# Kernel optimization log

Measured on AMD Instinct MI355X. Metric: run time of the kernel, lower is better.

The kernel has to match this reference:

```python
import jax, jax.numpy as jnp
import numpy as np

B, S, A, H, NH = 4, 4096, 512, 1024, 16
HD = H // NH  # 64


def setup_inputs() -> dict:
    key = jax.random.key(0)
    ks = jax.random.split(key, 12)
    s = 1.0 / np.sqrt(H)
    return {
        "hidden_states": jax.random.normal(ks[0], (B, S, H), jnp.float32),
        "audio_tokens": jax.random.normal(ks[1], (B, A, H), jnp.float32),
        "attention_mask": jax.random.randint(ks[2], (B, A), 0, 2, jnp.int32),
        "Wq": jax.random.normal(ks[3], (H, H), jnp.float32) * s,
        "bq": jnp.zeros((H,), jnp.float32),
        "Wk": jax.random.normal(ks[4], (H, H), jnp.float32) * s,
        "bk": jnp.zeros((H,), jnp.float32),
        "Wv": jax.random.normal(ks[5], (H, H), jnp.float32) * s,
        "bv": jnp.zeros((H,), jnp.float32),
        "Wo": jax.random.normal(ks[6], (H, H), jnp.float32) * s,
        "bo": jnp.zeros((H,), jnp.float32),
        "ln_gamma": jnp.ones((H,), jnp.float32),
        "ln_beta": jnp.zeros((H,), jnp.float32),
        "residual_scale": jnp.asarray(0.05, jnp.float32),
    }


def _san(x, big=10000.0):
    return jnp.nan_to_num(x, nan=0.0, posinf=big, neginf=-big)


def reference(hidden_states, audio_tokens, attention_mask, Wq, bq, Wk, bk, Wv, bv,
              Wo, bo, ln_gamma, ln_beta, residual_scale):
    hs = _san(hidden_states).astype(jnp.float32)
    at = _san(audio_tokens).astype(jnp.float32)

    def heads(x, W, b):  # [b, t, H] -> [b, t, nh, hd]
        return _san(x @ W.T + b).reshape(x.shape[0], x.shape[1], NH, HD)

    q = heads(hs, Wq, bq)            # [B,S,NH,HD]
    k = heads(at, Wk, bk)            # [B,A,NH,HD]
    v = heads(at, Wv, bv)            # [B,A,NH,HD]

    scale = max(np.sqrt(HD), 1e-8)
    scores = jnp.einsum("bsnd,band->bnsa", q, k) / scale  # [B,NH,S,A]
    scores = jnp.clip(_san(jnp.clip(scores, -50.0, 50.0), 50.0), -50.0, 50.0)

    attend = (attention_mask > 0)[:, None, None, :]       # [B,1,1,A]
    scores = jnp.where(attend, scores, -10000.0)
    scores = jnp.clip(scores, -50.0, 50.0)

    probs = jax.nn.softmax(scores, axis=-1)
    probs = _san(probs, 1.0)
    probs = probs / (jnp.sum(probs, axis=-1, keepdims=True) + 1e-8)

    ctx = jnp.einsum("bnsa,band->bsnd", probs, v).reshape(B, S, H)
    delta = _san(ctx @ Wo.T + bo)

    rs = jnp.clip(residual_scale, 0.0, 0.3)
    delta = rs * delta

    mu = jnp.mean(delta, axis=-1, keepdims=True)
    var = jnp.mean(jnp.square(delta - mu), axis=-1, keepdims=True)
    delta = (delta - mu) / jnp.sqrt(var + 1e-5) * ln_gamma + ln_beta
    return delta
```

## Files before the change

kernel.cpp:

```cpp
#include <hip/hip_runtime.h>
#include <hip/hip_bf16.h>
#include <cstdint>
#include <cstddef>

#define B_  4
#define S_  4096
#define A_  512
#define H_  1024
#define NH_ 16
#define HD_ 64

typedef __bf16 bf16;
typedef __bf16 bf16x8 __attribute__((ext_vector_type(8)));
typedef __bf16 bf16x4 __attribute__((ext_vector_type(4)));
typedef float  fx4    __attribute__((ext_vector_type(4)));

typedef __attribute__((address_space(3))) void LDS_v;
typedef const __attribute__((address_space(1))) void GLB_v;

__device__ __forceinline__ void gl_lds16(const void* g, void* l) {
    __builtin_amdgcn_global_load_lds((GLB_v*)g, (LDS_v*)l, 16, 0, 0);
}

__device__ __forceinline__ float sanf(float x) {
    if (x != x) return 0.f;
    if (fabsf(x) == __builtin_inff()) return x > 0.f ? 10000.f : -10000.f;
    return x;
}

__global__ __launch_bounds__(256) void cast_all(const float* __restrict__ hs,
                                                const float* __restrict__ at,
                                                const float* __restrict__ wq,
                                                const float* __restrict__ wk,
                                                const float* __restrict__ wv,
                                                const float* __restrict__ wo,
                                                bf16* __restrict__ dhs, bf16* __restrict__ dat,
                                                bf16* __restrict__ dwq, bf16* __restrict__ dwk,
                                                bf16* __restrict__ dwv, bf16* __restrict__ dwo) {
    int i = blockIdx.x * 256 + threadIdx.x;
    const float* s; bf16* d; int off;
    if (i < 4194304)      { s = hs; d = dhs; off = i; }
    else if (i < 4718592) { s = at; d = dat; off = i - 4194304; }
    else if (i < 4980736) { s = wq; d = dwq; off = i - 4718592; }
    else if (i < 5242880) { s = wk; d = dwk; off = i - 4980736; }
    else if (i < 5505024) { s = wv; d = dwv; off = i - 5242880; }
    else                  { s = wo; d = dwo; off = i - 5505024; }
    float4 v = ((const float4*)s)[off];
    bf16x4 o;
    o[0] = (bf16)sanf(v.x); o[1] = (bf16)sanf(v.y);
    o[2] = (bf16)sanf(v.z); o[3] = (bf16)sanf(v.w);
    *(bf16x4*)&d[(size_t)off * 4] = o;
}

__global__ __launch_bounds__(256) void qkv_gemm(const bf16* __restrict__ hsb,
                                                const bf16* __restrict__ atb,
                                                const bf16* __restrict__ wqb,
                                                const bf16* __restrict__ wkb,
                                                const bf16* __restrict__ wvb,
                                                const float* __restrict__ bq,
                                                const float* __restrict__ bk,
                                                const float* __restrict__ bv,
                                                bf16* __restrict__ Qb,
                                                bf16* __restrict__ Kb,
                                                bf16* __restrict__ Vtb) {
    __shared__ __align__(16) bf16 As[128 * 32];
    __shared__ __align__(16) bf16 Bs[128 * 32];

    const int id = blockIdx.x;
    int mode, m0, n0;
    const bf16 *A, *Bt; const float* bias;
    if (id < 1024)      { mode = 0; m0 = (id & 127) * 128; n0 = (id >> 7) * 128; A = hsb; Bt = wqb; bias = bq; }
    else if (id < 1152) { int t = id - 1024; mode = 1; m0 = (t & 15) * 128; n0 = (t >> 4) * 128; A = atb; Bt = wkb; bias = bk; }
    else                { int t = id - 1152; mode = 2; m0 = (t & 15) * 128; n0 = (t >> 4) * 128; A = atb; Bt = wvb; bias = bv; }

    const int tid  = threadIdx.x;
    const int lane = tid & 63;
    const int wv   = tid >> 6;
    const int wr   = wv >> 1, wc = wv & 1;
    const int lr   = lane & 15, kq = lane >> 4;

    fx4 acc[4][4] = {};

    const bf16* Ag = A  + (size_t)m0 * 1024;
    const bf16* Bg = Bt + (size_t)n0 * 1024;
    const int c0 = tid, c1 = tid + 256;
    const int row0 = c0 >> 2, kc0 = c0 & 3;
    const int row1 = c1 >> 2, kc1 = c1 & 3;

    for (int k0 = 0; k0 < 1024; k0 += 32) {
        gl_lds16(Ag + (size_t)row0 * 1024 + k0 + kc0 * 8, &As[c0 * 8]);
        gl_lds16(Ag + (size_t)row1 * 1024 + k0 + kc1 * 8, &As[c1 * 8]);
        gl_lds16(Bg + (size_t)row0 * 1024 + k0 + kc0 * 8, &Bs[c0 * 8]);
        gl_lds16(Bg + (size_t)row1 * 1024 + k0 + kc1 * 8, &Bs[c1 * 8]);
        __syncthreads();
        bf16x8 af[4], bfr[4];
#pragma unroll
        for (int i = 0; i < 4; i++) af[i]  = *(const bf16x8*)&As[(wr * 64 + i * 16 + lr) * 32 + kq * 8];
#pragma unroll
        for (int j = 0; j < 4; j++) bfr[j] = *(const bf16x8*)&Bs[(wc * 64 + j * 16 + lr) * 32 + kq * 8];
#pragma unroll
        for (int i = 0; i < 4; i++)
#pragma unroll
            for (int j = 0; j < 4; j++)
                acc[i][j] = __builtin_amdgcn_mfma_f32_16x16x32_bf16(af[i], bfr[j], acc[i][j], 0, 0, 0);
        __syncthreads();
    }

    float bb[4];
#pragma unroll
    for (int j = 0; j < 4; j++) bb[j] = bias[n0 + wc * 64 + j * 16 + lr];

    if (mode == 0) {
        const float sc = 0.18033688011112042f;
#pragma unroll
        for (int i = 0; i < 4; i++) {
            int row = m0 + wr * 64 + i * 16 + kq * 4;
#pragma unroll
            for (int j = 0; j < 4; j++) {
                int col = n0 + wc * 64 + j * 16 + lr;
#pragma unroll
                for (int r = 0; r < 4; r++)
                    Qb[(size_t)(row + r) * 1024 + col] = (bf16)((acc[i][j][r] + bb[j]) * sc);
            }
        }
    } else if (mode == 1) {
#pragma unroll
        for (int i = 0; i < 4; i++) {
            int row = m0 + wr * 64 + i * 16 + kq * 4;
#pragma unroll
            for (int j = 0; j < 4; j++) {
                int col = n0 + wc * 64 + j * 16 + lr;
#pragma unroll
                for (int r = 0; r < 4; r++)
                    Kb[(size_t)(row + r) * 1024 + col] = (bf16)(acc[i][j][r] + bb[j]);
            }
        }
    } else {
#pragma unroll
        for (int i = 0; i < 4; i++) {
            int m = m0 + wr * 64 + i * 16 + kq * 4;
            int bidx = m >> 9, a = m & 511;
#pragma unroll
            for (int j = 0; j < 4; j++) {
                int col = n0 + wc * 64 + j * 16 + lr;
                size_t base = ((size_t)bidx * H_ + col) * A_ + a;
#pragma unroll
                for (int r = 0; r < 4; r++)
                    Vtb[base + r] = (bf16)(acc[i][j][r] + bb[j]);
            }
        }
    }
}

__global__ __launch_bounds__(256) void gemm_o(const bf16* __restrict__ A,
                                              const bf16* __restrict__ Bt,
                                              const float* __restrict__ bias,
                                              float* __restrict__ C,
                                              const float* __restrict__ rsp) {
    __shared__ __align__(16) bf16 As[128 * 32];
    __shared__ __align__(16) bf16 Bs[128 * 32];

    const int tid  = threadIdx.x;
    const int lane = tid & 63;
    const int wv   = tid >> 6;
    const int wr   = wv >> 1, wc = wv & 1;
    const int lr   = lane & 15, kq = lane >> 4;
    const int m0   = blockIdx.x * 128, n0 = blockIdx.y * 128;

    fx4 acc[4][4] = {};

    const bf16* Ag = A  + (size_t)m0 * 1024;
    const bf16* Bg = Bt + (size_t)n0 * 1024;
    const int c0 = tid, c1 = tid + 256;
    const int row0 = c0 >> 2, kc0 = c0 & 3;
    const int row1 = c1 >> 2, kc1 = c1 & 3;

    for (int k0 = 0; k0 < 1024; k0 += 32) {
        gl_lds16(Ag + (size_t)row0 * 1024 + k0 + kc0 * 8, &As[c0 * 8]);
        gl_lds16(Ag + (size_t)row1 * 1024 + k0 + kc1 * 8, &As[c1 * 8]);
        gl_lds16(Bg + (size_t)row0 * 1024 + k0 + kc0 * 8, &Bs[c0 * 8]);
        gl_lds16(Bg + (size_t)row1 * 1024 + k0 + kc1 * 8, &Bs[c1 * 8]);
        __syncthreads();
        bf16x8 af[4], bfr[4];
#pragma unroll
        for (int i = 0; i < 4; i++) af[i]  = *(const bf16x8*)&As[(wr * 64 + i * 16 + lr) * 32 + kq * 8];
#pragma unroll
        for (int j = 0; j < 4; j++) bfr[j] = *(const bf16x8*)&Bs[(wc * 64 + j * 16 + lr) * 32 + kq * 8];
#pragma unroll
        for (int i = 0; i < 4; i++)
#pragma unroll
            for (int j = 0; j < 4; j++)
                acc[i][j] = __builtin_amdgcn_mfma_f32_16x16x32_bf16(af[i], bfr[j], acc[i][j], 0, 0, 0);
        __syncthreads();
    }

    float bb[4];
#pragma unroll
    for (int j = 0; j < 4; j++) bb[j] = bias[n0 + wc * 64 + j * 16 + lr];
    float rs = fminf(fmaxf(rsp[0], 0.f), 0.3f);
#pragma unroll
    for (int i = 0; i < 4; i++) {
        int row = m0 + wr * 64 + i * 16 + kq * 4;
#pragma unroll
        for (int j = 0; j < 4; j++) {
            int col = n0 + wc * 64 + j * 16 + lr;
#pragma unroll
            for (int r = 0; r < 4; r++)
                C[(size_t)(row + r) * 1024 + col] = rs * (acc[i][j][r] + bb[j]);
        }
    }
}

__global__ __launch_bounds__(256, 4) void attn_kernel(const bf16* __restrict__ Q,
                                                      const bf16* __restrict__ Kb,
                                                      const bf16* __restrict__ Vt,
                                                      const int* __restrict__ mask,
                                                      bf16* __restrict__ ctx) {
    __shared__ __align__(16) bf16 Qs[128 * 72];
    __shared__ __align__(16) bf16 Ks[64 * 72];
    __shared__ __align__(16) bf16 Vts[64 * 72];
    __shared__ float smask[512];
    __shared__ float dnm[128];

    const int tid  = threadIdx.x;
    const int lane = tid & 63;
    const int wv   = tid >> 6;
    const int lr   = lane & 15, kq = lane >> 4;
    const int st = blockIdx.x, h = blockIdx.y, b = blockIdx.z;
    const int m0 = b * S_ + st * 128;
    const float LO = -72.134752f;

    bf16x8 qtmp[4];
#pragma unroll
    for (int i = 0; i < 4; i++) {
        int c = tid + i * 256, row = c >> 3, ch = c & 7;
        qtmp[i] = *(const bf16x8*)(Q + (size_t)(m0 + row) * H_ + h * 64 + ch * 8);
    }
    smask[tid]       = (mask[b * A_ + tid] > 0)       ? -LO : LO;
    smask[tid + 256] = (mask[b * A_ + tid + 256] > 0) ? -LO : LO;
#pragma unroll
    for (int i = 0; i < 4; i++) {
        int c = tid + i * 256, row = c >> 3, ch = c & 7;
        *(bf16x8*)&Qs[row * 72 + ch * 8] = qtmp[i];
    }

    const int srow = tid >> 2, sseg = tid & 3;
    const size_t kg = (size_t)(b * A_ + srow) * H_ + h * 64 + sseg * 16;
    const size_t vg = (size_t)(b * H_ + h * 64 + srow) * A_ + sseg * 16;

    bf16x8 kr0 = *(const bf16x8*)(Kb + kg);
    bf16x8 kr1 = *(const bf16x8*)(Kb + kg + 8);
    bf16x8 vr0 = *(const bf16x8*)(Vt + vg);
    bf16x8 vr1 = *(const bf16x8*)(Vt + vg + 8);

    fx4 acco[2][4] = {};
    float dloc[2] = {0.f, 0.f};

    for (int it = 0; it < 8; it++) {
        const int a0 = it * 64;
        __syncthreads();
        *(bf16x8*)&Ks[srow * 72 + sseg * 16]      = kr0;
        *(bf16x8*)&Ks[srow * 72 + sseg * 16 + 8]  = kr1;
        *(bf16x8*)&Vts[srow * 72 + sseg * 16]     = vr0;
        *(bf16x8*)&Vts[srow * 72 + sseg * 16 + 8] = vr1;
        __syncthreads();

        if (it < 7) {
            const size_t ko = kg + (size_t)(a0 + 64) * H_;
            kr0 = *(const bf16x8*)(Kb + ko);
            kr1 = *(const bf16x8*)(Kb + ko + 8);
            vr0 = *(const bf16x8*)(Vt + vg + a0 + 64);
            vr1 = *(const bf16x8*)(Vt + vg + a0 + 64 + 8);
        }

        fx4 accs[4][2] = {};
#pragma unroll
        for (int kk = 0; kk < 64; kk += 32) {
            bf16x8 kf[4], qf[2];
#pragma unroll
            for (int mt = 0; mt < 4; mt++)
                kf[mt] = *(const bf16x8*)&Ks[(mt * 16 + lr) * 72 + kk + kq * 8];
#pragma unroll
            for (int nt = 0; nt < 2; nt++)
                qf[nt] = *(const bf16x8*)&Qs[(wv * 32 + nt * 16 + lr) * 72 + kk + kq * 8];
#pragma unroll
            for (int mt = 0; mt < 4; mt++)
#pragma unroll
                for (int nt = 0; nt < 2; nt++)
                    accs[mt][nt] = __builtin_amdgcn_mfma_f32_16x16x32_bf16(kf[mt], qf[nt], accs[mt][nt], 0, 0, 0);
        }

        bf16x4 pf[4][2];
#pragma unroll
        for (int mt = 0; mt < 4; mt++) {
            fx4 cap = *(const fx4*)&smask[a0 + mt * 16 + kq * 4];
#pragma unroll
            for (int nt = 0; nt < 2; nt++) {
#pragma unroll
                for (int r = 0; r < 4; r++) {
                    float s2 = fmaxf(fminf(accs[mt][nt][r], cap[r]), LO);
                    float p  = __builtin_amdgcn_exp2f(s2);
                    pf[mt][nt][r] = (bf16)p;
                    dloc[nt] += p;
                }
            }
        }

#pragma unroll
        for (int ks = 0; ks < 2; ks++) {
            bf16x8 pa[2];
#pragma unroll
            for (int stl = 0; stl < 2; stl++)
                pa[stl] = __builtin_shufflevector(pf[2 * ks][stl], pf[2 * ks + 1][stl],
                                                  0, 1, 2, 3, 4, 5, 6, 7);
#pragma unroll
            for (int dt = 0; dt < 4; dt++) {
                bf16x4 lo = *(const bf16x4*)&Vts[(dt * 16 + lr) * 72 + ks * 32 + kq * 4];
                bf16x4 hi = *(const bf16x4*)&Vts[(dt * 16 + lr) * 72 + ks * 32 + 16 + kq * 4];
                bf16x8 vf = __builtin_shufflevector(lo, hi, 0, 1, 2, 3, 4, 5, 6, 7);
#pragma unroll
                for (int stl = 0; stl < 2; stl++)
                    acco[stl][dt] = __builtin_amdgcn_mfma_f32_16x16x32_bf16(pa[stl], vf, acco[stl][dt], 0, 0, 0);
            }
        }
    }

#pragma unroll
    for (int nt = 0; nt < 2; nt++) {
        dloc[nt] += __shfl_xor(dloc[nt], 16);
        dloc[nt] += __shfl_xor(dloc[nt], 32);
    }
    if (kq == 0) {
        dnm[wv * 32 + lr]      = dloc[0];
        dnm[wv * 32 + 16 + lr] = dloc[1];
    }
    __syncthreads();

#pragma unroll
    for (int stl = 0; stl < 2; stl++) {
        fx4 dv = *(const fx4*)&dnm[wv * 32 + stl * 16 + kq * 4];
        float ri[4];
#pragma unroll
        for (int r = 0; r < 4; r++) ri[r] = __builtin_amdgcn_rcpf(dv[r]);
#pragma unroll
        for (int dt = 0; dt < 4; dt++)
#pragma unroll
            for (int r = 0; r < 4; r++)
                Qs[(wv * 32 + stl * 16 + kq * 4 + r) * 72 + dt * 16 + lr] =
                    (bf16)(acco[stl][dt][r] * ri[r]);
    }
    __syncthreads();
#pragma unroll
    for (int i = 0; i < 4; i++) {
        int c = tid + i * 256, row = c >> 3, ch = c & 7;
        *(bf16x8*)&ctx[(size_t)(m0 + row) * H_ + h * 64 + ch * 8] = *(const bf16x8*)&Qs[row * 72 + ch * 8];
    }
}

__global__ __launch_bounds__(256) void ln_kernel(float* __restrict__ io,
                                                 const float* __restrict__ gamma,
                                                 const float* __restrict__ beta) {
    __shared__ float red[8];
    const int tid = threadIdx.x;
    float4* rowp = (float4*)(io + (size_t)blockIdx.x * 1024);
    float4 x = rowp[tid];
    float s = x.x + x.y + x.z + x.w;
    float q = x.x * x.x + x.y * x.y + x.z * x.z + x.w * x.w;
#pragma unroll
    for (int off = 32; off > 0; off >>= 1) {
        s += __shfl_down(s, off);
        q += __shfl_down(q, off);
    }
    if ((tid & 63) == 0) { red[(tid >> 6) * 2] = s; red[(tid >> 6) * 2 + 1] = q; }
    __syncthreads();
    s = red[0] + red[2] + red[4] + red[6];
    q = red[1] + red[3] + red[5] + red[7];
    float mean = s * (1.f / 1024.f);
    float var  = q * (1.f / 1024.f) - mean * mean;
    float inv  = rsqrtf(var + 1e-5f);
    float4 g  = ((const float4*)gamma)[tid];
    float4 bb = ((const float4*)beta)[tid];
    float4 y;
    y.x = (x.x - mean) * inv * g.x + bb.x;
    y.y = (x.y - mean) * inv * g.y + bb.y;
    y.z = (x.z - mean) * inv * g.z + bb.z;
    y.w = (x.w - mean) * inv * g.w + bb.w;
    rowp[tid] = y;
}

extern "C" void kernel_launch(void* const* d_in, const int* in_sizes, int n_in,
                              void* d_out, int out_size, void* d_ws, size_t ws_size,
                              hipStream_t stream) {
    const float* hs    = (const float*)d_in[0];
    const float* at    = (const float*)d_in[1];
    const int*   maskp = (const int*)d_in[2];
    const float* Wq    = (const float*)d_in[3];
    const float* bq    = (const float*)d_in[4];
    const float* Wk    = (const float*)d_in[5];
    const float* bk    = (const float*)d_in[6];
    const float* Wv    = (const float*)d_in[7];
    const float* bv    = (const float*)d_in[8];
    const float* Wo    = (const float*)d_in[9];
    const float* bo    = (const float*)d_in[10];
    const float* gamma = (const float*)d_in[11];
    const float* beta  = (const float*)d_in[12];
    const float* rsp   = (const float*)d_in[13];

    char* ws = (char*)d_ws;
    bf16* hsb = (bf16*)(ws + 0);
    bf16* ctx = (bf16*)(ws + 0);
    bf16* atb = (bf16*)(ws + 33554432);
    bf16* wqb = (bf16*)(ws + 37748736);
    bf16* wkb = (bf16*)(ws + 39845888);
    bf16* wvb = (bf16*)(ws + 41943040);
    bf16* wob = (bf16*)(ws + 44040192);
    bf16* Qb  = (bf16*)(ws + 46137344);
    bf16* Kb  = (bf16*)(ws + 79691776);
    bf16* Vtb = (bf16*)(ws + 83886080);

    cast_all<<<22528, 256, 0, stream>>>(hs, at, Wq, Wk, Wv, Wo,
                                        hsb, atb, wqb, wkb, wvb, wob);

    qkv_gemm<<<1280, 256, 0, stream>>>(hsb, atb, wqb, wkb, wvb,
                                       bq, bk, bv, Qb, Kb, Vtb);

    attn_kernel<<<dim3(32, 16, 4), 256, 0, stream>>>(Qb, Kb, Vtb, maskp, ctx);

    gemm_o<<<dim3(128, 8), 256, 0, stream>>>(ctx, wob, bo, (float*)d_out, rsp);
    ln_kernel<<<16384, 256, 0, stream>>>((float*)d_out, gamma, beta);
}
```

Measured before the change: 329.3 us.

## Stage GEMM epilogues through LDS for coalesced stores and use bf16 intermediate

The Q/K and output-projection GEMM epilogues now write tiles into a padded shared-memory buffer and then issue coalesced 16-byte global stores, replacing scattered 2-byte stores. The V-transpose store is vectorized by permuting the A index order, and the attention kernel loads V in a matching permuted order so LDS fragments can be read as a single bf16x8. The output projection writes a bf16 intermediate that the LayerNorm kernel reads, halving that round-trip's traffic. The cost is an extra LDS pass and sync per tile, larger LDS use that may lower occupancy, and bf16 rounding of the pre-LayerNorm values.

```diff
diff --git a/kernel.cpp b/kernel.cpp
--- a/kernel.cpp
+++ b/kernel.cpp
@@ -17,6 +17,8 @@
 
 typedef __attribute__((address_space(3))) void LDS_v;
 typedef const __attribute__((address_space(1))) void GLB_v;
+
+#define CSTRIDE 136
 
 __device__ __forceinline__ void gl_lds16(const void* g, void* l) {
     __builtin_amdgcn_global_load_lds((GLB_v*)g, (LDS_v*)l, 16, 0, 0);
@@ -63,8 +65,10 @@
                                                 bf16* __restrict__ Qb,
                                                 bf16* __restrict__ Kb,
                                                 bf16* __restrict__ Vtb) {
-    __shared__ __align__(16) bf16 As[128 * 32];
-    __shared__ __align__(16) bf16 Bs[128 * 32];
+    __shared__ __align__(16) bf16 smem[128 * CSTRIDE];
+    bf16* As = smem;
+    bf16* Bs = smem + 128 * 32;
+    bf16* Cs = smem;
 
     const int id = blockIdx.x;
     int mode, m0, n0;
@@ -110,32 +114,7 @@
 #pragma unroll
     for (int j = 0; j < 4; j++) bb[j] = bias[n0 + wc * 64 + j * 16 + lr];
 
-    if (mode == 0) {
-        const float sc = 0.18033688011112042f;
-#pragma unroll
-        for (int i = 0; i < 4; i++) {
-            int row = m0 + wr * 64 + i * 16 + kq * 4;
-#pragma unroll
-            for (int j = 0; j < 4; j++) {
-                int col = n0 + wc * 64 + j * 16 + lr;
-#pragma unroll
-                for (int r = 0; r < 4; r++)
-                    Qb[(size_t)(row + r) * 1024 + col] = (bf16)((acc[i][j][r] + bb[j]) * sc);
-            }
-        }
-    } else if (mode == 1) {
-#pragma unroll
-        for (int i = 0; i < 4; i++) {
-            int row = m0 + wr * 64 + i * 16 + kq * 4;
-#pragma unroll
-            for (int j = 0; j < 4; j++) {
-                int col = n0 + wc * 64 + j * 16 + lr;
-#pragma unroll
-                for (int r = 0; r < 4; r++)
-                    Kb[(size_t)(row + r) * 1024 + col] = (bf16)(acc[i][j][r] + bb[j]);
-            }
-        }
-    } else {
+    if (mode == 2) {
 #pragma unroll
         for (int i = 0; i < 4; i++) {
             int m = m0 + wr * 64 + i * 16 + kq * 4;
@@ -143,11 +122,31 @@
 #pragma unroll
             for (int j = 0; j < 4; j++) {
                 int col = n0 + wc * 64 + j * 16 + lr;
-                size_t base = ((size_t)bidx * H_ + col) * A_ + a;
+                bf16x4 o;
+#pragma unroll
+                for (int r = 0; r < 4; r++) o[r] = (bf16)(acc[i][j][r] + bb[j]);
+                *(bf16x4*)&Vtb[((size_t)bidx * H_ + col) * A_ + a] = o;
+            }
+        }
+    } else {
+        const float sc = (mode == 0) ? 0.18033688011112042f : 1.0f;
+#pragma unroll
+        for (int i = 0; i < 4; i++) {
+            int rowb = wr * 64 + i * 16 + kq * 4;
+#pragma unroll
+            for (int j = 0; j < 4; j++) {
+                int col = wc * 64 + j * 16 + lr;
 #pragma unroll
                 for (int r = 0; r < 4; r++)
-                    Vtb[base + r] = (bf16)(acc[i][j][r] + bb[j]);
+                    Cs[(rowb + r) * CSTRIDE + col] = (bf16)((acc[i][j][r] + bb[j]) * sc);
             }
+        }
+        __syncthreads();
+        bf16* outp = (mode == 0) ? Qb : Kb;
+#pragma unroll
+        for (int p = 0; p < 8; p++) {
+            int c = tid + p * 256, row = c >> 4, cc = (c & 15) * 8;
+            *(bf16x8*)&outp[(size_t)(m0 + row) * 1024 + n0 + cc] = *(const bf16x8*)&Cs[row * CSTRIDE + cc];
         }
     }
 }
@@ -155,10 +154,12 @@
 __global__ __launch_bounds__(256) void gemm_o(const bf16* __restrict__ A,
                                               const bf16* __restrict__ Bt,
                                               const float* __restrict__ bias,
-                                              float* __restrict__ C,
+                                              bf16* __restrict__ C,
                                               const float* __restrict__ rsp) {
-    __shared__ __align__(16) bf16 As[128 * 32];
-    __shared__ __align__(16) bf16 Bs[128 * 32];
+    __shared__ __align__(16) bf16 smem[128 * CSTRIDE];
+    bf16* As = smem;
+    bf16* Bs = smem + 128 * 32;
+    bf16* Cs = smem;
 
     const int tid  = threadIdx.x;
     const int lane = tid & 63;
@@ -198,16 +199,23 @@
 #pragma unroll
     for (int j = 0; j < 4; j++) bb[j] = bias[n0 + wc * 64 + j * 16 + lr];
     float rs = fminf(fmaxf(rsp[0], 0.f), 0.3f);
+
 #pragma unroll
     for (int i = 0; i < 4; i++) {
-        int row = m0 + wr * 64 + i * 16 + kq * 4;
+        int rowb = wr * 64 + i * 16 + kq * 4;
 #pragma unroll
         for (int j = 0; j < 4; j++) {
-            int col = n0 + wc * 64 + j * 16 + lr;
+            int col = wc * 64 + j * 16 + lr;
 #pragma unroll
             for (int r = 0; r < 4; r++)
-                C[(size_t)(row + r) * 1024 + col] = rs * (acc[i][j][r] + bb[j]);
-        }
+                Cs[(rowb + r) * CSTRIDE + col] = (bf16)(rs * (acc[i][j][r] + bb[j]));
+        }
+    }
+    __syncthreads();
+#pragma unroll
+    for (int p = 0; p < 8; p++) {
+        int c = tid + p * 256, row = c >> 4, cc = (c & 15) * 8;
+        *(bf16x8*)&C[(size_t)(m0 + row) * 1024 + n0 + cc] = *(const bf16x8*)&Cs[row * CSTRIDE + cc];
     }
 }
 
@@ -246,12 +254,16 @@
 
     const int srow = tid >> 2, sseg = tid & 3;
     const size_t kg = (size_t)(b * A_ + srow) * H_ + h * 64 + sseg * 16;
-    const size_t vg = (size_t)(b * H_ + h * 64 + srow) * A_ + sseg * 16;
+    const bf16* vrow = Vt + (size_t)(b * H_ + h * 64 + srow) * A_;
+    const int va0 = 32 * (sseg >> 1) + 4 * ((2 * sseg) & 3);
+    const int va1 = 32 * (sseg >> 1) + 4 * ((2 * sseg + 1) & 3);
 
     bf16x8 kr0 = *(const bf16x8*)(Kb + kg);
     bf16x8 kr1 = *(const bf16x8*)(Kb + kg + 8);
-    bf16x8 vr0 = *(const bf16x8*)(Vt + vg);
-    bf16x8 vr1 = *(const bf16x8*)(Vt + vg + 8);
+    bf16x4 v00 = *(const bf16x4*)(vrow + va0);
+    bf16x4 v01 = *(const bf16x4*)(vrow + va0 + 16);
+    bf16x4 v10 = *(const bf16x4*)(vrow + va1);
+    bf16x4 v11 = *(const bf16x4*)(vrow + va1 + 16);
 
     fx4 acco[2][4] = {};
     float dloc[2] = {0.f, 0.f};
@@ -261,16 +273,20 @@
         __syncthreads();
         *(bf16x8*)&Ks[srow * 72 + sseg * 16]      = kr0;
         *(bf16x8*)&Ks[srow * 72 + sseg * 16 + 8]  = kr1;
-        *(bf16x8*)&Vts[srow * 72 + sseg * 16]     = vr0;
-        *(bf16x8*)&Vts[srow * 72 + sseg * 16 + 8] = vr1;
+        *(bf16x8*)&Vts[srow * 72 + sseg * 16] =
+            __builtin_shufflevector(v00, v01, 0, 1, 2, 3, 4, 5, 6, 7);
+        *(bf16x8*)&Vts[srow * 72 + sseg * 16 + 8] =
+            __builtin_shufflevector(v10, v11, 0, 1, 2, 3, 4, 5, 6, 7);
         __syncthreads();
 
         if (it < 7) {
             const size_t ko = kg + (size_t)(a0 + 64) * H_;
             kr0 = *(const bf16x8*)(Kb + ko);
             kr1 = *(const bf16x8*)(Kb + ko + 8);
-            vr0 = *(const bf16x8*)(Vt + vg + a0 + 64);
-            vr1 = *(const bf16x8*)(Vt + vg + a0 + 64 + 8);
+            v00 = *(const bf16x4*)(vrow + a0 + 64 + va0);
+            v01 = *(const bf16x4*)(vrow + a0 + 64 + va0 + 16);
+            v10 = *(const bf16x4*)(vrow + a0 + 64 + va1);
+            v11 = *(const bf16x4*)(vrow + a0 + 64 + va1 + 16);
         }
 
         fx4 accs[4][2] = {};
@@ -315,9 +331,7 @@
                                                   0, 1, 2, 3, 4, 5, 6, 7);
 #pragma unroll
             for (int dt = 0; dt < 4; dt++) {
-                bf16x4 lo = *(const bf16x4*)&Vts[(dt * 16 + lr) * 72 + ks * 32 + kq * 4];
-                bf16x4 hi = *(const bf16x4*)&Vts[(dt * 16 + lr) * 72 + ks * 32 + 16 + kq * 4];
-                bf16x8 vf = __builtin_shufflevector(lo, hi, 0, 1, 2, 3, 4, 5, 6, 7);
+                bf16x8 vf = *(const bf16x8*)&Vts[(dt * 16 + lr) * 72 + ks * 32 + kq * 8];
 #pragma unroll
                 for (int stl = 0; stl < 2; stl++)
                     acco[stl][dt] = __builtin_amdgcn_mfma_f32_16x16x32_bf16(pa[stl], vf, acco[stl][dt], 0, 0, 0);
@@ -357,15 +371,16 @@
     }
 }
 
-__global__ __launch_bounds__(256) void ln_kernel(float* __restrict__ io,
+__global__ __launch_bounds__(256) void ln_kernel(const bf16* __restrict__ in,
+                                                 float* __restrict__ out,
                                                  const float* __restrict__ gamma,
                                                  const float* __restrict__ beta) {
     __shared__ float red[8];
     const int tid = threadIdx.x;
-    float4* rowp = (float4*)(io + (size_t)blockIdx.x * 1024);
-    float4 x = rowp[tid];
-    float s = x.x + x.y + x.z + x.w;
-    float q = x.x * x.x + x.y * x.y + x.z * x.z + x.w * x.w;
+    bf16x4 xb = *(const bf16x4*)&in[(size_t)blockIdx.x * 1024 + tid * 4];
+    float x0 = (float)xb[0], x1 = (float)xb[1], x2 = (float)xb[2], x3 = (float)xb[3];
+    float s = x0 + x1 + x2 + x3;
+    float q = x0 * x0 + x1 * x1 + x2 * x2 + x3 * x3;
 #pragma unroll
     for (int off = 32; off > 0; off >>= 1) {
         s += __shfl_down(s, off);
@@ -381,11 +396,11 @@
     float4 g  = ((const float4*)gamma)[tid];
     float4 bb = ((const float4*)beta)[tid];
     float4 y;
-    y.x = (x.x - mean) * inv * g.x + bb.x;
-    y.y = (x.y - mean) * inv * g.y + bb.y;
-    y.z = (x.z - mean) * inv * g.z + bb.z;
-    y.w = (x.w - mean) * inv * g.w + bb.w;
-    rowp[tid] = y;
+    y.x = (x0 - mean) * inv * g.x + bb.x;
+    y.y = (x1 - mean) * inv * g.y + bb.y;
+    y.z = (x2 - mean) * inv * g.z + bb.z;
+    y.w = (x3 - mean) * inv * g.w + bb.w;
+    ((float4*)(out + (size_t)blockIdx.x * 1024))[tid] = y;
 }
 
 extern "C" void kernel_launch(void* const* d_in, const int* in_sizes, int n_in,
@@ -415,6 +430,7 @@
     bf16* wvb = (bf16*)(ws + 41943040);
     bf16* wob = (bf16*)(ws + 44040192);
     bf16* Qb  = (bf16*)(ws + 46137344);
+    bf16* Ob  = Qb;
     bf16* Kb  = (bf16*)(ws + 79691776);
     bf16* Vtb = (bf16*)(ws + 83886080);
 
@@ -426,6 +442,6 @@
 
     attn_kernel<<<dim3(32, 16, 4), 256, 0, stream>>>(Qb, Kb, Vtb, maskp, ctx);
 
-    gemm_o<<<dim3(128, 8), 256, 0, stream>>>(ctx, wob, bo, (float*)d_out, rsp);
-    ln_kernel<<<16384, 256, 0, stream>>>((float*)d_out, gamma, beta);
-}
+    gemm_o<<<dim3(128, 8), 256, 0, stream>>>(ctx, wob, bo, Ob, rsp);
+    ln_kernel<<<16384, 256, 0, stream>>>(Ob, (float*)d_out, gamma, beta);
+}
```

Result: no change. 327.8 us (-0.5%).
